# Kernel optimization log

Hardware: AMD Instinct MI355X
Metric: run time of the kernel (lower is better)

## Reference

```python
import jax, jax.numpy as jnp
import numpy as np

B, T, V, E, H = 64, 32, 32000, 512, 1024  # batch, caption len, vocab, embed, hidden


def setup_inputs() -> dict:
    key = jax.random.key(0)
    ks = jax.random.split(key, 10)
    sV = 1.0 / np.sqrt(V)   # nn.Linear init scale
    sH = 1.0 / np.sqrt(H)   # nn.LSTM init scale
    return {
        "features": jax.random.normal(ks[0], (B, E), jnp.float32),
        "captions": jax.random.randint(ks[1], (B, T), 0, V, dtype=jnp.int32),
        # embed = nn.Linear(vocab_size, embed_size): W [E, V], b [E]
        "W_embed": jax.random.uniform(ks[2], (E, V), jnp.float32, -sV, sV),
        "b_embed": jax.random.uniform(ks[3], (E,), jnp.float32, -sV, sV),
        # single-layer LSTM params, PyTorch gate order (i, f, g, o)
        "w_ih": jax.random.uniform(ks[4], (4 * H, E), jnp.float32, -sH, sH),
        "w_hh": jax.random.uniform(ks[5], (4 * H, H), jnp.float32, -sH, sH),
        "b_ih": jax.random.uniform(ks[6], (4 * H,), jnp.float32, -sH, sH),
        "b_hh": jax.random.uniform(ks[7], (4 * H,), jnp.float32, -sH, sH),
        # the torch module draws these with torch.randn at every call; made explicit here
        "h0": jax.random.normal(ks[8], (B, H), jnp.float32),
        "c0": jax.random.normal(ks[9], (B, H), jnp.float32),
    }


def _lstm(inputs, h0, c0, w_ih, w_hh, b_ih, b_hh):
    # inputs: [B, S, E] -> outputs [B, S, H]
    def step(carry, x_t):
        h, c = carry
        gates = x_t @ w_ih.T + h @ w_hh.T + (b_ih + b_hh)  # [B, 4H]
        i, f, g, o = jnp.split(gates, 4, axis=-1)
        c = jax.nn.sigmoid(f) * c + jax.nn.sigmoid(i) * jnp.tanh(g)
        h = jax.nn.sigmoid(o) * jnp.tanh(c)
        return (h, c), h

    _, hs = jax.lax.scan(step, (h0, c0), jnp.transpose(inputs, (1, 0, 2)))
    return jnp.transpose(hs, (1, 0, 2))


def reference(features, captions, W_embed, b_embed, w_ih, w_hh, b_ih, b_hh, h0, c0):
    # Faithful to the original: expand captions to dense one-hot [B, T, V]
    # and push through the Linear layer (the exact wasteful op pattern under study).
    onehot = jax.nn.one_hot(captions, V, dtype=jnp.float32)       # [B, T, V]
    emb = jnp.einsum("btv,ev->bte", onehot, W_embed) + b_embed     # [B, T, E]
    inputs = jnp.concatenate([features[:, None, :], emb], axis=1)  # [B, T+1, E]
    return _lstm(inputs, h0, c0, w_ih, w_hh, b_ih, b_hh)           # [B, T+1, H]
```

## Files before the change

kernel.cpp:

```cpp
#include <hip/hip_runtime.h>
#include <hip/hip_bf16.h>

#define B_   64
#define T_   32
#define S_   33
#define V_   32000
#define E_   512
#define H_   1024
#define HB_  (B_ * H_)
#define NG_  4096

typedef __attribute__((ext_vector_type(8))) short  bf16x8;
typedef __attribute__((ext_vector_type(4))) float  f32x4;

__device__ inline void split2(float x, unsigned short& hi, unsigned short& lo) {
    __hip_bfloat16 h = __float2bfloat16(x);
    float r = x - __bfloat162float(h);
    __hip_bfloat16 l = __float2bfloat16(r);
    hi = *reinterpret_cast<unsigned short*>(&h);
    lo = *reinterpret_cast<unsigned short*>(&l);
}

__device__ inline void load_f32x8_hilo(const float* __restrict__ p,
                                       bf16x8& hi, bf16x8& lo) {
    const float4* q = reinterpret_cast<const float4*>(p);
    float4 v0 = q[0], v1 = q[1];
    float f[8] = {v0.x, v0.y, v0.z, v0.w, v1.x, v1.y, v1.z, v1.w};
#pragma unroll
    for (int j = 0; j < 8; ++j) {
        unsigned short h, l; split2(f[j], h, l);
        hi[j] = (short)h; lo[j] = (short)l;
    }
}

__device__ inline void load_hpk8(const unsigned int* __restrict__ p,
                                 bf16x8& hi, bf16x8& lo) {
    uint4 v0 = *reinterpret_cast<const uint4*>(p);
    uint4 v1 = *reinterpret_cast<const uint4*>(p + 4);
    unsigned int w[8] = {v0.x, v0.y, v0.z, v0.w, v1.x, v1.y, v1.z, v1.w};
#pragma unroll
    for (int j = 0; j < 8; ++j) {
        hi[j] = (short)(w[j] & 0xffffu);
        lo[j] = (short)(w[j] >> 16);
    }
}

__global__ __launch_bounds__(512) void build_x(
    const float* __restrict__ feat,
    const int*   __restrict__ caps,
    const float* __restrict__ Wemb,
    const float* __restrict__ bemb,
    unsigned short* __restrict__ Xhi,
    unsigned short* __restrict__ Xlo)
{
    int row = blockIdx.x;
    int t = row >> 6, b = row & 63;
    int e = threadIdx.x;
    float x;
    if (t == 0) {
        x = feat[b * E_ + e];
    } else {
        int cap = caps[b * T_ + (t - 1)];
        x = Wemb[(size_t)e * V_ + cap] + bemb[e];
    }
    unsigned short hi, lo; split2(x, hi, lo);
    Xhi[(size_t)row * E_ + e] = hi;
    Xlo[(size_t)row * E_ + e] = lo;
}

__global__ __launch_bounds__(256) void init_state(
    const float* __restrict__ h0,
    const float* __restrict__ c0,
    unsigned int* __restrict__ hseq0,
    float* __restrict__ c,
    unsigned int* __restrict__ flags,
    unsigned int* __restrict__ gen)
{
    int idx = blockIdx.x * 256 + threadIdx.x;
    if (idx < 512 * 32) flags[idx] = 0u;
    if (idx < 128)      gen[idx]   = 0u;
    unsigned short hi, lo; split2(h0[idx], hi, lo);
    hseq0[idx] = (unsigned int)hi | ((unsigned int)lo << 16);
    c[idx]   = c0[idx];
}

__global__ __launch_bounds__(256) void split_w(
    const float* __restrict__ src,
    unsigned short* __restrict__ hi,
    unsigned short* __restrict__ lo,
    int n4)
{
    int idx = blockIdx.x * 256 + threadIdx.x;
    int stride = gridDim.x * 256;
    for (; idx < n4; idx += stride) {
        float4 v = reinterpret_cast<const float4*>(src)[idx];
        float f[4] = {v.x, v.y, v.z, v.w};
        unsigned short h[4], l[4];
#pragma unroll
        for (int j = 0; j < 4; ++j) split2(f[j], h[j], l[j]);
        ushort4 hv; hv.x = h[0]; hv.y = h[1]; hv.z = h[2]; hv.w = h[3];
        ushort4 lv; lv.x = l[0]; lv.y = l[1]; lv.z = l[2]; lv.w = l[3];
        *reinterpret_cast<ushort4*>(hi + (size_t)idx * 4) = hv;
        *reinterpret_cast<ushort4*>(lo + (size_t)idx * 4) = lv;
    }
}

__global__ __launch_bounds__(256) void bias_sum(
    const float* __restrict__ a, const float* __restrict__ b,
    float* __restrict__ s)
{
    int i = blockIdx.x * 256 + threadIdx.x;
    s[i] = a[i] + b[i];
}

template<bool PRESPLIT>
__global__ __launch_bounds__(256) void gx_gemm(
    const unsigned short* __restrict__ Xhi,
    const unsigned short* __restrict__ Xlo,
    const unsigned short* __restrict__ Wihhi,
    const unsigned short* __restrict__ Wihlo,
    const float* __restrict__ w_ih,
    const float* __restrict__ bsum,
    float* __restrict__ Gxi)
{
    int bx   = blockIdx.x;
    int jg   = bx & 255;
    int m0   = (bx >> 8) * 32;
    int wave = threadIdx.x >> 6;
    int lane = threadIdx.x & 63;
    int lm   = lane & 15;
    int kq   = (lane >> 4) * 8;
    int tid  = threadIdx.x;
    int nrow = (lm >> 2) * H_ + jg * 4 + (lm & 3);
    int k0   = wave * 128;

    const unsigned short* Bhi = nullptr;
    const unsigned short* Blo = nullptr;
    const float* Bf = nullptr;
    if (PRESPLIT) { Bhi = Wihhi + (size_t)nrow * E_; Blo = Wihlo + (size_t)nrow * E_; }
    else          { Bf  = w_ih + (size_t)nrow * E_; }

    f32x4 acc0 = f32x4{0.f, 0.f, 0.f, 0.f};
    f32x4 acc1 = f32x4{0.f, 0.f, 0.f, 0.f};

#pragma unroll
    for (int kk = 0; kk < 128; kk += 32) {
        int k = k0 + kk + kq;
        bf16x8 bhi, blo;
        if constexpr (PRESPLIT) {
            bhi = *reinterpret_cast<const bf16x8*>(Bhi + k);
            blo = *reinterpret_cast<const bf16x8*>(Blo + k);
        } else {
            load_f32x8_hilo(Bf + k, bhi, blo);
        }
        bf16x8 a0h = *reinterpret_cast<const bf16x8*>(Xhi + (size_t)(m0 + lm) * E_ + k);
        bf16x8 a0l = *reinterpret_cast<const bf16x8*>(Xlo + (size_t)(m0 + lm) * E_ + k);
        bf16x8 a1h = *reinterpret_cast<const bf16x8*>(Xhi + (size_t)(m0 + 16 + lm) * E_ + k);
        bf16x8 a1l = *reinterpret_cast<const bf16x8*>(Xlo + (size_t)(m0 + 16 + lm) * E_ + k);
        acc0 = __builtin_amdgcn_mfma_f32_16x16x32_bf16(a0h, bhi, acc0, 0, 0, 0);
        acc0 = __builtin_amdgcn_mfma_f32_16x16x32_bf16(a0l, bhi, acc0, 0, 0, 0);
        acc0 = __builtin_amdgcn_mfma_f32_16x16x32_bf16(a0h, blo, acc0, 0, 0, 0);
        acc1 = __builtin_amdgcn_mfma_f32_16x16x32_bf16(a1h, bhi, acc1, 0, 0, 0);
        acc1 = __builtin_amdgcn_mfma_f32_16x16x32_bf16(a1l, bhi, acc1, 0, 0, 0);
        acc1 = __builtin_amdgcn_mfma_f32_16x16x32_bf16(a1h, blo, acc1, 0, 0, 0);
    }

    __shared__ float pbuf[4][2][16][17];
    int rbase = (lane >> 4) * 4;
#pragma unroll
    for (int r = 0; r < 4; ++r) {
        pbuf[wave][0][rbase + r][lm] = acc0[r];
        pbuf[wave][1][rbase + r][lm] = acc1[r];
    }
    __syncthreads();

    for (int idx = tid; idx < 512; idx += 256) {
        int mt = idx >> 8, rc = idx & 255;
        int row = rc >> 4, col = rc & 15;
        float v = pbuf[0][mt][row][col] + pbuf[1][mt][row][col]
                + pbuf[2][mt][row][col] + pbuf[3][mt][row][col];
        int n = (col >> 2) * H_ + jg * 4 + (col & 3);
        Gxi[(size_t)(m0 + mt * 16 + row) * NG_ + jg * 16 + col] = v + bsum[n];
    }
}

template<bool PRESPLIT>
__global__ __launch_bounds__(256, 2) void lstm_persist(
    const float* __restrict__ Gxi,
    const unsigned short* __restrict__ Whhhi,
    const unsigned short* __restrict__ Whhlo,
    const float* __restrict__ w_hh,
    unsigned int* __restrict__ hseq,
    float* __restrict__ c,
    float* __restrict__ out,
    unsigned int* __restrict__ flags,
    unsigned int* __restrict__ gen)
{
    int bx   = blockIdx.x;
    int jg   = bx & 255;
    int mgrp = bx >> 8;
    int wave = threadIdx.x >> 6;
    int lane = threadIdx.x & 63;
    int lm   = lane & 15;
    int kq   = (lane >> 4) * 8;
    int tid  = threadIdx.x;

    int gbase    = bx & 256;
    bool checker = (bx == gbase);
    unsigned int* mygen = gen + (mgrp * 64);

    int nrow = (lm >> 2) * H_ + jg * 4 + (lm & 3);
    int k0   = wave * 256;

    const unsigned short* Bhi = nullptr;
    const unsigned short* Blo = nullptr;
    const float* Bf = nullptr;
    if (PRESPLIT) { Bhi = Whhhi + (size_t)nrow * H_; Blo = Whhlo + (size_t)nrow * H_; }
    else          { Bf  = w_hh + (size_t)nrow * H_; }

    __shared__ float pbuf[4][2][16][17];
    __shared__ float gbuf[2][16][17];
    int rbase = (lane >> 4) * 4;

    for (int t = 0; t < S_; ++t) {
        const unsigned int* hpk_in = hseq + (size_t)t * HB_;
        unsigned int*      hpk_out = hseq + (size_t)(t + 1) * HB_;
        const unsigned int* hrow0 = hpk_in + (size_t)(mgrp * 32 + lm) * H_;
        const unsigned int* hrow1 = hpk_in + (size_t)(mgrp * 32 + 16 + lm) * H_;

        f32x4 acc0 = f32x4{0.f, 0.f, 0.f, 0.f};
        f32x4 acc1 = f32x4{0.f, 0.f, 0.f, 0.f};

#pragma unroll
        for (int kk = 0; kk < 256; kk += 32) {
            int k = k0 + kk + kq;
            bf16x8 bhi, blo;
            if constexpr (PRESPLIT) {
                bhi = *reinterpret_cast<const bf16x8*>(Bhi + k);
                blo = *reinterpret_cast<const bf16x8*>(Blo + k);
            } else {
                load_f32x8_hilo(Bf + k, bhi, blo);
            }
            bf16x8 a0h, a0l, a1h, a1l;
            load_hpk8(hrow0 + k, a0h, a0l);
            load_hpk8(hrow1 + k, a1h, a1l);
            acc0 = __builtin_amdgcn_mfma_f32_16x16x32_bf16(a0h, bhi, acc0, 0, 0, 0);
            acc0 = __builtin_amdgcn_mfma_f32_16x16x32_bf16(a0l, bhi, acc0, 0, 0, 0);
            acc0 = __builtin_amdgcn_mfma_f32_16x16x32_bf16(a0h, blo, acc0, 0, 0, 0);
            acc1 = __builtin_amdgcn_mfma_f32_16x16x32_bf16(a1h, bhi, acc1, 0, 0, 0);
            acc1 = __builtin_amdgcn_mfma_f32_16x16x32_bf16(a1l, bhi, acc1, 0, 0, 0);
            acc1 = __builtin_amdgcn_mfma_f32_16x16x32_bf16(a1h, blo, acc1, 0, 0, 0);
        }

#pragma unroll
        for (int r = 0; r < 4; ++r) {
            pbuf[wave][0][rbase + r][lm] = acc0[r];
            pbuf[wave][1][rbase + r][lm] = acc1[r];
        }
        __syncthreads();

        for (int idx = tid; idx < 512; idx += 256) {
            int mt = idx >> 8, rc = idx & 255;
            int row = rc >> 4, col = rc & 15;
            gbuf[mt][row][col] = pbuf[0][mt][row][col] + pbuf[1][mt][row][col]
                               + pbuf[2][mt][row][col] + pbuf[3][mt][row][col];
        }
        __syncthreads();

        if (tid < 128) {
            int mt = tid >> 6, bl = (tid >> 2) & 15, jj = tid & 3;
            int b = mgrp * 32 + mt * 16 + bl;
            int j = jg * 4 + jj;
            const float* gx = Gxi + (size_t)(t * 64 + b) * NG_ + jg * 16;
            float iv = gbuf[mt][bl][ 0 + jj] + gx[ 0 + jj];
            float fv = gbuf[mt][bl][ 4 + jj] + gx[ 4 + jj];
            float gv = gbuf[mt][bl][ 8 + jj] + gx[ 8 + jj];
            float ov = gbuf[mt][bl][12 + jj] + gx[12 + jj];
            float si = 1.f / (1.f + expf(-iv));
            float sf = 1.f / (1.f + expf(-fv));
            float so = 1.f / (1.f + expf(-ov));
            float tg = tanhf(gv);
            size_t cidx = (size_t)b * H_ + j;
            float cn = sf * c[cidx] + si * tg;
            c[cidx] = cn;
            float hn = so * tanhf(cn);
            unsigned short hi, lo; split2(hn, hi, lo);
            __hip_atomic_store(&hpk_out[cidx],
                               (unsigned int)hi | ((unsigned int)lo << 16),
                               __ATOMIC_RELAXED, __HIP_MEMORY_SCOPE_AGENT);
            out[((size_t)b * S_ + t) * H_ + j] = hn;
        }

        __syncthreads();
        unsigned int target = (unsigned int)(t + 1);
        if (!checker) {
            if (tid == 0) {
                __hip_atomic_store(&flags[(size_t)bx * 32], target,
                                   __ATOMIC_RELAXED, __HIP_MEMORY_SCOPE_AGENT);
                while (__hip_atomic_load(mygen, __ATOMIC_RELAXED,
                                         __HIP_MEMORY_SCOPE_AGENT) < target) {
                    __builtin_amdgcn_s_sleep(2);
                }
            }
        } else {
            int fi = gbase + 1 + tid;
            bool need = (tid < 255);
            for (;;) {
                int ok = 1;
                if (need) {
                    ok = (__hip_atomic_load(&flags[(size_t)fi * 32],
                                            __ATOMIC_RELAXED,
                                            __HIP_MEMORY_SCOPE_AGENT) >= target);
                }
                if (__syncthreads_and(ok)) break;
                __builtin_amdgcn_s_sleep(2);
            }
            if (tid == 0) {
                __hip_atomic_store(mygen, target,
                                   __ATOMIC_RELAXED, __HIP_MEMORY_SCOPE_AGENT);
            }
        }
        __syncthreads();
    }
}

template<bool PRESPLIT>
__global__ __launch_bounds__(256) void lstm_step(
    const float* __restrict__ Gxi,
    const unsigned short* __restrict__ Whhhi,
    const unsigned short* __restrict__ Whhlo,
    const float* __restrict__ w_hh,
    const unsigned int* __restrict__ hpk_in,
    float* __restrict__ c,
    unsigned int* __restrict__ hpk_out,
    float* __restrict__ out,
    int t)
{
    int bx   = blockIdx.x;
    int jg   = bx & 255;
    int mgrp = bx >> 8;
    int wave = threadIdx.x >> 6;
    int lane = threadIdx.x & 63;
    int lm   = lane & 15;
    int kq   = (lane >> 4) * 8;
    int tid  = threadIdx.x;
    int nrow = (lm >> 2) * H_ + jg * 4 + (lm & 3);
    int k0   = wave * 256;

    const unsigned short* Bhi = nullptr;
    const unsigned short* Blo = nullptr;
    const float* Bf = nullptr;
    if (PRESPLIT) { Bhi = Whhhi + (size_t)nrow * H_; Blo = Whhlo + (size_t)nrow * H_; }
    else          { Bf  = w_hh + (size_t)nrow * H_; }

    const unsigned int* hrow0 = hpk_in + (size_t)(mgrp * 32 + lm) * H_;
    const unsigned int* hrow1 = hpk_in + (size_t)(mgrp * 32 + 16 + lm) * H_;

    f32x4 acc0 = f32x4{0.f, 0.f, 0.f, 0.f};
    f32x4 acc1 = f32x4{0.f, 0.f, 0.f, 0.f};

#pragma unroll
    for (int kk = 0; kk < 256; kk += 32) {
        int k = k0 + kk + kq;
        bf16x8 bhi, blo;
        if constexpr (PRESPLIT) {
            bhi = *reinterpret_cast<const bf16x8*>(Bhi + k);
            blo = *reinterpret_cast<const bf16x8*>(Blo + k);
        } else {
            load_f32x8_hilo(Bf + k, bhi, blo);
        }
        bf16x8 a0h, a0l, a1h, a1l;
        load_hpk8(hrow0 + k, a0h, a0l);
        load_hpk8(hrow1 + k, a1h, a1l);
        acc0 = __builtin_amdgcn_mfma_f32_16x16x32_bf16(a0h, bhi, acc0, 0, 0, 0);
        acc0 = __builtin_amdgcn_mfma_f32_16x16x32_bf16(a0l, bhi, acc0, 0, 0, 0);
        acc0 = __builtin_amdgcn_mfma_f32_16x16x32_bf16(a0h, blo, acc0, 0, 0, 0);
        acc1 = __builtin_amdgcn_mfma_f32_16x16x32_bf16(a1h, bhi, acc1, 0, 0, 0);
        acc1 = __builtin_amdgcn_mfma_f32_16x16x32_bf16(a1l, bhi, acc1, 0, 0, 0);
        acc1 = __builtin_amdgcn_mfma_f32_16x16x32_bf16(a1h, blo, acc1, 0, 0, 0);
    }

    __shared__ float pbuf[4][2][16][17];
    __shared__ float gbuf[2][16][17];
    int rbase = (lane >> 4) * 4;
#pragma unroll
    for (int r = 0; r < 4; ++r) {
        pbuf[wave][0][rbase + r][lm] = acc0[r];
        pbuf[wave][1][rbase + r][lm] = acc1[r];
    }
    __syncthreads();

    for (int idx = tid; idx < 512; idx += 256) {
        int mt = idx >> 8, rc = idx & 255;
        int row = rc >> 4, col = rc & 15;
        gbuf[mt][row][col] = pbuf[0][mt][row][col] + pbuf[1][mt][row][col]
                           + pbuf[2][mt][row][col] + pbuf[3][mt][row][col];
    }
    __syncthreads();

    if (tid < 128) {
        int mt = tid >> 6, bl = (tid >> 2) & 15, jj = tid & 3;
        int b = mgrp * 32 + mt * 16 + bl;
        int j = jg * 4 + jj;
        const float* gx = Gxi + (size_t)(t * 64 + b) * NG_ + jg * 16;
        float iv = gbuf[mt][bl][ 0 + jj] + gx[ 0 + jj];
        float fv = gbuf[mt][bl][ 4 + jj] + gx[ 4 + jj];
        float gv = gbuf[mt][bl][ 8 + jj] + gx[ 8 + jj];
        float ov = gbuf[mt][bl][12 + jj] + gx[12 + jj];
        float si = 1.f / (1.f + expf(-iv));
        float sf = 1.f / (1.f + expf(-fv));
        float so = 1.f / (1.f + expf(-ov));
        float tg = tanhf(gv);
        size_t cidx = (size_t)b * H_ + j;
        float cn = sf * c[cidx] + si * tg;
        c[cidx] = cn;
        float hn = so * tanhf(cn);
        unsigned short hi, lo; split2(hn, hi, lo);
        hpk_out[cidx] = (unsigned int)hi | ((unsigned int)lo << 16);
        out[((size_t)b * S_ + t) * H_ + j] = hn;
    }
}

extern "C" void kernel_launch(void* const* d_in, const int* in_sizes, int n_in,
                              void* d_out, int out_size, void* d_ws, size_t ws_size,
                              hipStream_t stream)
{
    const float* feat = (const float*)d_in[0];
    const int*   caps = (const int*)d_in[1];
    const float* Wemb = (const float*)d_in[2];
    const float* bemb = (const float*)d_in[3];
    const float* w_ih = (const float*)d_in[4];
    const float* w_hh = (const float*)d_in[5];
    const float* b_ih = (const float*)d_in[6];
    const float* b_hh = (const float*)d_in[7];
    const float* h0   = (const float*)d_in[8];
    const float* c0   = (const float*)d_in[9];
    int nbias = 0, nstate = 0;
    for (int i = 0; i < n_in; ++i) {
        switch (in_sizes[i]) {
            case 64 * 512:        feat = (const float*)d_in[i]; break;
            case 64 * 32:         caps = (const int*)d_in[i];   break;
            case 512 * 32000:     Wemb = (const float*)d_in[i]; break;
            case 512:             bemb = (const float*)d_in[i]; break;
            case 4096 * 512:      w_ih = (const float*)d_in[i]; break;
            case 4096 * 1024:     w_hh = (const float*)d_in[i]; break;
            case 4096:
                if (nbias++ == 0) b_ih = (const float*)d_in[i];
                else              b_hh = (const float*)d_in[i];
                break;
            case 64 * 1024:
                if (nstate++ == 0) h0 = (const float*)d_in[i];
                else               c0 = (const float*)d_in[i];
                break;
            default: break;
        }
    }
    float* out = (float*)d_out;

    char* ws = (char*)d_ws;
    unsigned short* Xhi  = (unsigned short*)ws; ws += (size_t)2112 * 512 * 2;
    unsigned short* Xlo  = (unsigned short*)ws; ws += (size_t)2112 * 512 * 2;
    float* Gxi           = (float*)ws;          ws += (size_t)2112 * NG_ * 4;
    unsigned int* hseq   = (unsigned int*)ws;   ws += (size_t)(S_ + 1) * HB_ * 4;
    float* cbuf          = (float*)ws;          ws += (size_t)B_ * H_ * 4;
    float* bsum          = (float*)ws;          ws += (size_t)4096 * 4;
    unsigned int* flags  = (unsigned int*)ws;   ws += (size_t)512 * 32 * 4;
    unsigned int* gen    = (unsigned int*)ws;   ws += (size_t)128 * 4;
    unsigned short* Wihhi = (unsigned short*)ws; ws += (size_t)4096 * 512 * 2;
    unsigned short* Wihlo = (unsigned short*)ws; ws += (size_t)4096 * 512 * 2;
    unsigned short* Whhhi = (unsigned short*)ws; ws += (size_t)4096 * 1024 * 2;
    unsigned short* Whhlo = (unsigned short*)ws; ws += (size_t)4096 * 1024 * 2;
    size_t needed = (size_t)(ws - (char*)d_ws);
    bool presplit = ws_size >= needed;

    build_x<<<2112, 512, 0, stream>>>(feat, caps, Wemb, bemb, Xhi, Xlo);
    init_state<<<256, 256, 0, stream>>>(h0, c0, hseq, cbuf, flags, gen);
    bias_sum<<<16, 256, 0, stream>>>(b_ih, b_hh, bsum);
    if (presplit) {
        split_w<<<2048, 256, 0, stream>>>(w_ih, Wihhi, Wihlo, (4096 * 512) / 4);
        split_w<<<2048, 256, 0, stream>>>(w_hh, Whhhi, Whhlo, (4096 * 1024) / 4);
        gx_gemm<true><<<66 * 256, 256, 0, stream>>>(Xhi, Xlo, Wihhi, Wihlo,
                                                    w_ih, bsum, Gxi);
    } else {
        gx_gemm<false><<<66 * 256, 256, 0, stream>>>(Xhi, Xlo, Wihhi, Wihlo,
                                                     w_ih, bsum, Gxi);
    }

    void* args[] = {
        (void*)&Gxi,
        (void*)&Whhhi, (void*)&Whhlo, (void*)&w_hh,
        (void*)&hseq, (void*)&cbuf, (void*)&out,
        (void*)&flags, (void*)&gen
    };
    const void* pk = presplit ? (const void*)lstm_persist<true>
                              : (const void*)lstm_persist<false>;
    hipError_t err = hipLaunchCooperativeKernel(pk, dim3(512), dim3(256),
                                                args, 0, stream);
    if (err != hipSuccess) {
        (void)hipGetLastError();
        for (int t = 0; t < S_; ++t) {
            const unsigned int* hin = hseq + (size_t)t * HB_;
            unsigned int*      hout = hseq + (size_t)(t + 1) * HB_;
            if (presplit) {
                lstm_step<true><<<512, 256, 0, stream>>>(
                    Gxi, Whhhi, Whhlo, w_hh, hin, cbuf, hout, out, t);
            } else {
                lstm_step<false><<<512, 256, 0, stream>>>(
                    Gxi, Whhhi, Whhlo, w_hh, hin, cbuf, hout, out, t);
            }
        }
    }
}
```

Baseline: 720.3 us.

## Keep W_hh slices in registers and spread generation flags across cache lines

Each block of the persistent recurrent kernel now loads its W_hh hi/lo slice into registers once, before the time loop, instead of reloading it from memory every step. The Gx input-gate values are prefetched before the MFMA loop so their latency overlaps the matmul. The single per-group generation counter becomes 64 counters on separate cache lines, each polled by 4 blocks and written by 64 threads of the checker, which should cut contention on the barrier. The cost is higher register pressure (16 bf16x8 vectors per thread) and a larger workspace for gen, which could lower occupancy or cause spills.

Measured after the change: 695.7 us. 1.04x faster.

```diff
diff --git a/kernel.cpp b/kernel.cpp
--- a/kernel.cpp
+++ b/kernel.cpp
@@ -77,8 +77,8 @@
     unsigned int* __restrict__ gen)
 {
     int idx = blockIdx.x * 256 + threadIdx.x;
-    if (idx < 512 * 32) flags[idx] = 0u;
-    if (idx < 128)      gen[idx]   = 0u;
+    if (idx < 512 * 32)  flags[idx] = 0u;
+    if (idx < 2 * 64 * 32) gen[idx] = 0u;
     unsigned short hi, lo; split2(h0[idx], hi, lo);
     hseq0[idx] = (unsigned int)hi | ((unsigned int)lo << 16);
     c[idx]   = c0[idx];
@@ -207,16 +207,27 @@
 
     int gbase    = bx & 256;
     bool checker = (bx == gbase);
-    unsigned int* mygen = gen + (mgrp * 64);
+    unsigned int* mygen = gen + ((size_t)mgrp * 64 + ((bx & 255) >> 2)) * 32;
 
     int nrow = (lm >> 2) * H_ + jg * 4 + (lm & 3);
     int k0   = wave * 256;
 
-    const unsigned short* Bhi = nullptr;
-    const unsigned short* Blo = nullptr;
-    const float* Bf = nullptr;
-    if (PRESPLIT) { Bhi = Whhhi + (size_t)nrow * H_; Blo = Whhlo + (size_t)nrow * H_; }
-    else          { Bf  = w_hh + (size_t)nrow * H_; }
+    bf16x8 wh[8], wl[8];
+    if constexpr (PRESPLIT) {
+        const unsigned short* Bhi = Whhhi + (size_t)nrow * H_ + k0 + kq;
+        const unsigned short* Blo = Whhlo + (size_t)nrow * H_ + k0 + kq;
+#pragma unroll
+        for (int i = 0; i < 8; ++i) {
+            wh[i] = *reinterpret_cast<const bf16x8*>(Bhi + i * 32);
+            wl[i] = *reinterpret_cast<const bf16x8*>(Blo + i * 32);
+        }
+    } else {
+        const float* Bf = w_hh + (size_t)nrow * H_ + k0 + kq;
+#pragma unroll
+        for (int i = 0; i < 8; ++i) {
+            load_f32x8_hilo(Bf + i * 32, wh[i], wl[i]);
+        }
+    }
 
     __shared__ float pbuf[4][2][16][17];
     __shared__ float gbuf[2][16][17];
@@ -225,31 +236,34 @@
     for (int t = 0; t < S_; ++t) {
         const unsigned int* hpk_in = hseq + (size_t)t * HB_;
         unsigned int*      hpk_out = hseq + (size_t)(t + 1) * HB_;
-        const unsigned int* hrow0 = hpk_in + (size_t)(mgrp * 32 + lm) * H_;
-        const unsigned int* hrow1 = hpk_in + (size_t)(mgrp * 32 + 16 + lm) * H_;
+        const unsigned int* hrow0 = hpk_in + (size_t)(mgrp * 32 + lm) * H_ + k0 + kq;
+        const unsigned int* hrow1 = hpk_in + (size_t)(mgrp * 32 + 16 + lm) * H_ + k0 + kq;
+
+        float gx_i = 0.f, gx_f = 0.f, gx_g = 0.f, gx_o = 0.f;
+        if (tid < 128) {
+            int mt = tid >> 6, bl = (tid >> 2) & 15, jj = tid & 3;
+            int b = mgrp * 32 + mt * 16 + bl;
+            const float* gx = Gxi + (size_t)(t * 64 + b) * NG_ + jg * 16;
+            gx_i = gx[ 0 + jj];
+            gx_f = gx[ 4 + jj];
+            gx_g = gx[ 8 + jj];
+            gx_o = gx[12 + jj];
+        }
 
         f32x4 acc0 = f32x4{0.f, 0.f, 0.f, 0.f};
         f32x4 acc1 = f32x4{0.f, 0.f, 0.f, 0.f};
 
 #pragma unroll
-        for (int kk = 0; kk < 256; kk += 32) {
-            int k = k0 + kk + kq;
-            bf16x8 bhi, blo;
-            if constexpr (PRESPLIT) {
-                bhi = *reinterpret_cast<const bf16x8*>(Bhi + k);
-                blo = *reinterpret_cast<const bf16x8*>(Blo + k);
-            } else {
-                load_f32x8_hilo(Bf + k, bhi, blo);
-            }
+        for (int i = 0; i < 8; ++i) {
             bf16x8 a0h, a0l, a1h, a1l;
-            load_hpk8(hrow0 + k, a0h, a0l);
-            load_hpk8(hrow1 + k, a1h, a1l);
-            acc0 = __builtin_amdgcn_mfma_f32_16x16x32_bf16(a0h, bhi, acc0, 0, 0, 0);
-            acc0 = __builtin_amdgcn_mfma_f32_16x16x32_bf16(a0l, bhi, acc0, 0, 0, 0);
-            acc0 = __builtin_amdgcn_mfma_f32_16x16x32_bf16(a0h, blo, acc0, 0, 0, 0);
-            acc1 = __builtin_amdgcn_mfma_f32_16x16x32_bf16(a1h, bhi, acc1, 0, 0, 0);
-            acc1 = __builtin_amdgcn_mfma_f32_16x16x32_bf16(a1l, bhi, acc1, 0, 0, 0);
-            acc1 = __builtin_amdgcn_mfma_f32_16x16x32_bf16(a1h, blo, acc1, 0, 0, 0);
+            load_hpk8(hrow0 + i * 32, a0h, a0l);
+            load_hpk8(hrow1 + i * 32, a1h, a1l);
+            acc0 = __builtin_amdgcn_mfma_f32_16x16x32_bf16(a0h, wh[i], acc0, 0, 0, 0);
+            acc0 = __builtin_amdgcn_mfma_f32_16x16x32_bf16(a0l, wh[i], acc0, 0, 0, 0);
+            acc0 = __builtin_amdgcn_mfma_f32_16x16x32_bf16(a0h, wl[i], acc0, 0, 0, 0);
+            acc1 = __builtin_amdgcn_mfma_f32_16x16x32_bf16(a1h, wh[i], acc1, 0, 0, 0);
+            acc1 = __builtin_amdgcn_mfma_f32_16x16x32_bf16(a1l, wh[i], acc1, 0, 0, 0);
+            acc1 = __builtin_amdgcn_mfma_f32_16x16x32_bf16(a1h, wl[i], acc1, 0, 0, 0);
         }
 
 #pragma unroll
@@ -271,11 +285,10 @@
             int mt = tid >> 6, bl = (tid >> 2) & 15, jj = tid & 3;
             int b = mgrp * 32 + mt * 16 + bl;
             int j = jg * 4 + jj;
-            const float* gx = Gxi + (size_t)(t * 64 + b) * NG_ + jg * 16;
-            float iv = gbuf[mt][bl][ 0 + jj] + gx[ 0 + jj];
-            float fv = gbuf[mt][bl][ 4 + jj] + gx[ 4 + jj];
-            float gv = gbuf[mt][bl][ 8 + jj] + gx[ 8 + jj];
-            float ov = gbuf[mt][bl][12 + jj] + gx[12 + jj];
+            float iv = gbuf[mt][bl][ 0 + jj] + gx_i;
+            float fv = gbuf[mt][bl][ 4 + jj] + gx_f;
+            float gv = gbuf[mt][bl][ 8 + jj] + gx_g;
+            float ov = gbuf[mt][bl][12 + jj] + gx_o;
             float si = 1.f / (1.f + expf(-iv));
             float sf = 1.f / (1.f + expf(-fv));
             float so = 1.f / (1.f + expf(-ov));
@@ -315,8 +328,8 @@
                 if (__syncthreads_and(ok)) break;
                 __builtin_amdgcn_s_sleep(2);
             }
-            if (tid == 0) {
-                __hip_atomic_store(mygen, target,
+            if (tid < 64) {
+                __hip_atomic_store(gen + ((size_t)mgrp * 64 + tid) * 32, target,
                                    __ATOMIC_RELAXED, __HIP_MEMORY_SCOPE_AGENT);
             }
         }
@@ -465,7 +478,7 @@
     float* cbuf          = (float*)ws;          ws += (size_t)B_ * H_ * 4;
     float* bsum          = (float*)ws;          ws += (size_t)4096 * 4;
     unsigned int* flags  = (unsigned int*)ws;   ws += (size_t)512 * 32 * 4;
-    unsigned int* gen    = (unsigned int*)ws;   ws += (size_t)128 * 4;
+    unsigned int* gen    = (unsigned int*)ws;   ws += (size_t)2 * 64 * 32 * 4;
     unsigned short* Wihhi = (unsigned short*)ws; ws += (size_t)4096 * 512 * 2;
     unsigned short* Wihlo = (unsigned short*)ws; ws += (size_t)4096 * 512 * 2;
     unsigned short* Whhhi = (unsigned short*)ws; ws += (size_t)4096 * 1024 * 2;
```
